# Optimization experiments

Hardware: AMD Instinct MI355X
Metric: run time of the kernel (lower is better)

The kernel has to match this reference:

```python
import jax, jax.numpy as jnp
import numpy as np

N = 100_000   # nodes
E = 1_600_000 # edges
D = 32        # input_channels
H = 32        # hidden_inputs
C = 8         # output_channels
G = 64        # graphs in batch


def setup_inputs() -> dict:
    key = jax.random.key(0)
    ks = jax.random.split(key, 12)
    inp = {
        "x": jax.random.normal(ks[0], (N, D), dtype=jnp.float32),
        "edge_idx": jax.random.randint(ks[1], (2, E), 0, N, dtype=jnp.int64 if jax.config.jax_enable_x64 else jnp.int32),
        "edge_weight": jax.random.uniform(ks[2], (E,), dtype=jnp.float32),
        "batch": jnp.sort(jax.random.randint(ks[3], (N,), 0, G, dtype=jnp.int32)),
        # GCNConv weights (PyG: out = A_hat @ (x W) + b)
        "W1": jax.random.normal(ks[4], (D, H), dtype=jnp.float32) / np.sqrt(D),
        "b1": jnp.zeros((H,), dtype=jnp.float32),
        "W2": jax.random.normal(ks[5], (H, H), dtype=jnp.float32) / np.sqrt(H),
        "b2": jnp.zeros((H,), dtype=jnp.float32),
        "W3": jax.random.normal(ks[6], (H, H), dtype=jnp.float32) / np.sqrt(H),
        "b3": jnp.zeros((H,), dtype=jnp.float32),
        "Wout": jax.random.normal(ks[7], (H, C), dtype=jnp.float32) / np.sqrt(H),
        "bout": jnp.zeros((C,), dtype=jnp.float32),
    }
    return inp


def _gcn_norm(edge_idx, edge_weight, n_nodes):
    """Add self-loops (weight 1) and compute symmetric normalization,
    matching torch_geometric gcn_norm(add_self_loops=True)."""
    loop = jnp.arange(n_nodes, dtype=edge_idx.dtype)
    row = jnp.concatenate([edge_idx[0], loop])          # source j
    col = jnp.concatenate([edge_idx[1], loop])          # target i
    w = jnp.concatenate([edge_weight, jnp.ones((n_nodes,), edge_weight.dtype)])
    deg = jax.ops.segment_sum(w, col, num_segments=n_nodes)  # in-degree of targets
    dinv = jnp.where(deg > 0, jax.lax.rsqrt(deg), 0.0)
    norm = dinv[row] * w * dinv[col]
    return row, col, norm


def _gcn_conv(x, W, b, row, col, norm, n_nodes):
    h = x @ W                                   # [N, H] small GEMM
    msg = h[row] * norm[:, None]                # gather + scale  [E+N, H]
    agg = jax.ops.segment_sum(msg, col, num_segments=n_nodes)  # scatter-add
    return agg + b


def reference(x, edge_idx, edge_weight, batch, W1, b1, W2, b2, W3, b3, Wout, bout):
    n = x.shape[0]
    row, col, norm = _gcn_norm(edge_idx, edge_weight, n)
    h = jax.nn.relu(_gcn_conv(x, W1, b1, row, col, norm, n))
    h = jax.nn.relu(_gcn_conv(h, W2, b2, row, col, norm, n))
    h = jax.nn.relu(_gcn_conv(h, W3, b3, row, col, norm, n))
    # global mean pool over graphs
    sums = jax.ops.segment_sum(h, batch, num_segments=G)          # [G, H]
    cnts = jax.ops.segment_sum(jnp.ones((n,), h.dtype), batch, num_segments=G)
    pooled = sums / jnp.maximum(cnts, 1.0)[:, None]
    # dropout is identity in eval mode
    logits = pooled @ Wout + bout
    return jax.nn.log_softmax(logits, axis=1)
```

## Files before the change

kernel.cpp:

```cpp
#include <hip/hip_runtime.h>
#include <math.h>

#define NN 100000
#define NE 1600000
#define HD 32
#define NG 64
#define NC 8

#define P 256
#define PART 391
#define SCAP 7000
#define CH 8192
#define NBIN ((NE + CH - 1) / CH)
#define NORM_BLOCKS (NN * 8 / 256)
#define GEMM0_BLOCKS (NN / 8)

__device__ __forceinline__ float bf2f(unsigned short u) {
    return __uint_as_float(((unsigned int)u) << 16);
}
__device__ __forceinline__ unsigned short f2bf(float f) {
    unsigned int b = __float_as_uint(f);
    b = (b + 0x7FFFu + ((b >> 16) & 1u)) >> 16;
    return (unsigned short)b;
}

#if __has_builtin(__builtin_amdgcn_cvt_pk_f32_fp8) && __has_builtin(__builtin_amdgcn_cvt_pk_fp8_f32)
#define FP8_HW 1
#else
#define FP8_HW 0
#endif

__device__ __forceinline__ float e4m3f_sw(unsigned u) {
    unsigned code = u & 0x7fu;
    unsigned e = code >> 3;
    float v;
    if (e == 0) v = (float)code * 0.001953125f;
    else v = __uint_as_float(((e + 120u) << 23) | ((code & 7u) << 20));
    return (u & 0x80u) ? -v : v;
}
__device__ __forceinline__ unsigned f2e4m3_sw(float f) {
    unsigned s = (__float_as_uint(f) >> 31) << 7;
    float a = fminf(fabsf(f), 448.0f);
    unsigned code;
    if (a >= 0.015625f) {
        unsigned x = __float_as_uint(a);
        x += 0x0007FFFFu + ((x >> 20) & 1u);
        code = (((x >> 23) - 120u) << 3) | ((x >> 20) & 7u);
    } else {
        code = (unsigned)__float2int_rn(a * 512.0f);
    }
    return s | code;
}

__device__ __forceinline__ float4 fp8x4f(unsigned v) {
#if FP8_HW
    using floatx2 = __attribute__((ext_vector_type(2))) float;
    floatx2 lo = __builtin_amdgcn_cvt_pk_f32_fp8((int)v, false);
    floatx2 hi = __builtin_amdgcn_cvt_pk_f32_fp8((int)v, true);
    return make_float4(lo[0], lo[1], hi[0], hi[1]);
#else
    return make_float4(e4m3f_sw(v & 255), e4m3f_sw((v >> 8) & 255),
                       e4m3f_sw((v >> 16) & 255), e4m3f_sw(v >> 24));
#endif
}
__device__ __forceinline__ unsigned f4fp8(float a, float b, float c, float d) {
#if FP8_HW
    int pk = 0;
    pk = __builtin_amdgcn_cvt_pk_fp8_f32(a, b, pk, false);
    pk = __builtin_amdgcn_cvt_pk_fp8_f32(c, d, pk, true);
    return (unsigned)pk;
#else
    return f2e4m3_sw(a) | (f2e4m3_sw(b) << 8) | (f2e4m3_sw(c) << 16) | (f2e4m3_sw(d) << 24);
#endif
}
__device__ __forceinline__ unsigned char f1fp8(float a) {
#if FP8_HW
    return (unsigned char)(__builtin_amdgcn_cvt_pk_fp8_f32(a, a, 0, false) & 0xff);
#else
    return (unsigned char)f2e4m3_sw(a);
#endif
}

__global__ __launch_bounds__(1024) void k_bin(const int* __restrict__ row,
                                              const int* __restrict__ col,
                                              const float* __restrict__ w,
                                              int* __restrict__ pcnt,
                                              uint2* __restrict__ staging) {
    __shared__ int scol[CH];
    __shared__ int hist[P];
    __shared__ int base_[P];
    int tid = threadIdx.x;
    int e0 = blockIdx.x * CH;
    int nrem = min(CH, NE - e0);
    if (tid < P) hist[tid] = 0;
    __syncthreads();
    for (int i = tid; i < nrem; i += 1024) {
        int c = col[e0 + i];
        scol[i] = c;
        atomicAdd(&hist[(unsigned)c / PART], 1);
    }
    __syncthreads();
    if (tid < P) {
        int h = hist[tid];
        base_[tid] = h ? atomicAdd(&pcnt[tid], h) : 0;
        hist[tid] = 0;
    }
    __syncthreads();
    for (int i = tid; i < nrem; i += 1024) {
        int c = scol[i];
        int p = (unsigned)c / PART;
        int pos = base_[p] + atomicAdd(&hist[p], 1);
        uint2 v;
        v.x = (unsigned)(c - p * PART) | ((unsigned)row[e0 + i] << 9);
        v.y = __float_as_uint(w[e0 + i]);
        staging[(size_t)p * SCAP + pos] = v;
    }
}

__global__ __launch_bounds__(256) void k_csrA_gemm0(const int* __restrict__ pcnt,
                                                    const uint2* __restrict__ staging,
                                                    int* __restrict__ off,
                                                    int* __restrict__ cntg,
                                                    float* __restrict__ dinv,
                                                    const float* __restrict__ x,
                                                    const float* __restrict__ W1,
                                                    unsigned char* __restrict__ h1) {
    int tid = threadIdx.x;
    if (blockIdx.x < P) {
        __shared__ int spc[P];
        __shared__ int cnt_l[PART];
        __shared__ float wsum[PART];
        __shared__ int sc[PART];
        int p = blockIdx.x;
        spc[tid] = pcnt[tid];
        __syncthreads();
#pragma unroll
        for (int d = 1; d < P; d <<= 1) {
            int t = (tid >= d) ? spc[tid - d] : 0;
            __syncthreads();
            spc[tid] += t;
            __syncthreads();
        }
        int m = pcnt[p];
        int pb = (p > 0) ? spc[p - 1] : 0;
        for (int i = tid; i < PART; i += 256) { cnt_l[i] = 0; wsum[i] = 0.0f; }
        __syncthreads();
        const uint2* st = staging + (size_t)p * SCAP;
        for (int i = tid; i < m; i += 256) {
            uint2 v = st[i];
            int cl = v.x & 511;
            atomicAdd(&cnt_l[cl], 1);
            atomicAdd(&wsum[cl], __uint_as_float(v.y));
        }
        __syncthreads();
        for (int i = tid; i < PART; i += 256) sc[i] = cnt_l[i];
        __syncthreads();
        int i0 = tid, i1 = tid + 256;
#pragma unroll
        for (int d = 1; d < 512; d <<= 1) {
            int t0 = 0, t1 = 0;
            if (i0 < PART && i0 >= d) t0 = sc[i0 - d];
            if (i1 < PART && i1 >= d) t1 = sc[i1 - d];
            __syncthreads();
            if (i0 < PART) sc[i0] += t0;
            if (i1 < PART) sc[i1] += t1;
            __syncthreads();
        }
        for (int i = tid; i < PART; i += 256) {
            int n = p * PART + i;
            if (n < NN) {
                off[n] = pb + sc[i] - cnt_l[i];
                cntg[n] = cnt_l[i];
                dinv[n] = rsqrtf(1.0f + wsum[i]);
            }
        }
    } else {
        __shared__ float sW[32 * 32];
        __shared__ float sX[8 * 32];
        int base = (blockIdx.x - P) * 8;
        ((float4*)sW)[tid] = ((const float4*)W1)[tid];
        if (tid < 64) ((float4*)sX)[tid] = ((const float4*)(x + (size_t)base * 32))[tid];
        __syncthreads();
        int c = tid & 31, nl = tid >> 5;
        float acc = 0.0f;
#pragma unroll
        for (int k = 0; k < 32; ++k) acc = fmaf(sX[nl * 32 + k], sW[k * 32 + c], acc);
        h1[(size_t)(base + nl) * 32 + c] = f1fp8(acc);
    }
}

__global__ __launch_bounds__(512) void k_csr_b(const int* __restrict__ pcnt,
                                               const uint2* __restrict__ staging,
                                               const int* __restrict__ off,
                                               const float* __restrict__ dinv,
                                               unsigned* __restrict__ pairs) {
    __shared__ int cur[PART];
    __shared__ float sdc[PART];
    int p = blockIdx.x, tid = threadIdx.x;
    int m = pcnt[p];
    const uint2* st = staging + (size_t)p * SCAP;
    for (int i = tid; i < PART; i += 512) {
        int n = p * PART + i;
        cur[i] = (n < NN) ? off[n] : 0;
        sdc[i] = (n < NN) ? dinv[n] : 0.0f;
    }
    __syncthreads();
    for (int ib = tid; ib < m; ib += 512 * 4) {
        uint2 v[4];
        float dr[4];
#pragma unroll
        for (int j = 0; j < 4; ++j) {
            int i = ib + j * 512;
            if (i < m) v[j] = st[i];
        }
#pragma unroll
        for (int j = 0; j < 4; ++j) {
            int i = ib + j * 512;
            if (i < m) dr[j] = dinv[v[j].x >> 9];
        }
#pragma unroll
        for (int j = 0; j < 4; ++j) {
            int i = ib + j * 512;
            if (i < m) {
                int cl = v[j].x & 511;
                int pos = atomicAdd(&cur[cl], 1);
                float y = dr[j] * __uint_as_float(v[j].y) * sdc[cl];
                unsigned q = (unsigned)__float2int_rn(y * 32768.0f);
                q = min(q, 32767u);
                pairs[pos] = ((v[j].x >> 9) << 15) | q;
            }
        }
    }
}

#define NM_SCALE 3.0517578125e-5f
template <int MODE>
__global__ __launch_bounds__(256) void k_gather(const unsigned char* __restrict__ hb,
                                                const int* __restrict__ off,
                                                const int* __restrict__ cntg,
                                                const float* __restrict__ dinv,
                                                const unsigned* __restrict__ pairs,
                                                const float* __restrict__ bias,
                                                const float* __restrict__ Wn,
                                                unsigned char* __restrict__ hout,
                                                unsigned short* __restrict__ h3out) {
    __shared__ float sW[32 * 32];
    __shared__ float srow[32 * 33];
    int tid = threadIdx.x;
    if (MODE == 0) ((float4*)sW)[tid] = ((const float4*)Wn)[tid];
    int t = blockIdx.x * 256 + tid;
    int n = t >> 3, c4 = t & 7;
    int cn = cntg[n];
    const unsigned* pp = pairs + off[n];
    float di = dinv[n], sl = di * di;
    unsigned hu = *(const unsigned*)(hb + (size_t)n * 32 + c4 * 4);
    float4 hf = fp8x4f(hu);
    float4 acc = make_float4(sl * hf.x, sl * hf.y, sl * hf.z, sl * hf.w);
    int k = 0;
    for (; k + 8 <= cn; k += 8) {
        unsigned p[8];
#pragma unroll
        for (int j = 0; j < 8; ++j) p[j] = pp[k + j];
        unsigned v[8];
#pragma unroll
        for (int j = 0; j < 8; ++j)
            v[j] = *(const unsigned*)(hb + (size_t)(p[j] >> 15) * 32 + c4 * 4);
#pragma unroll
        for (int j = 0; j < 8; ++j) {
            float nm = (float)(p[j] & 32767u) * NM_SCALE;
            float4 f = fp8x4f(v[j]);
            acc.x = fmaf(nm, f.x, acc.x);
            acc.y = fmaf(nm, f.y, acc.y);
            acc.z = fmaf(nm, f.z, acc.z);
            acc.w = fmaf(nm, f.w, acc.w);
        }
    }
    for (; k + 4 <= cn; k += 4) {
        unsigned p[4];
#pragma unroll
        for (int j = 0; j < 4; ++j) p[j] = pp[k + j];
        unsigned v[4];
#pragma unroll
        for (int j = 0; j < 4; ++j)
            v[j] = *(const unsigned*)(hb + (size_t)(p[j] >> 15) * 32 + c4 * 4);
#pragma unroll
        for (int j = 0; j < 4; ++j) {
            float nm = (float)(p[j] & 32767u) * NM_SCALE;
            float4 f = fp8x4f(v[j]);
            acc.x = fmaf(nm, f.x, acc.x);
            acc.y = fmaf(nm, f.y, acc.y);
            acc.z = fmaf(nm, f.z, acc.z);
            acc.w = fmaf(nm, f.w, acc.w);
        }
    }
    for (; k < cn; ++k) {
        unsigned p = pp[k];
        unsigned v = *(const unsigned*)(hb + (size_t)(p >> 15) * 32 + c4 * 4);
        float nm = (float)(p & 32767u) * NM_SCALE;
        float4 f = fp8x4f(v);
        acc.x = fmaf(nm, f.x, acc.x);
        acc.y = fmaf(nm, f.y, acc.y);
        acc.z = fmaf(nm, f.z, acc.z);
        acc.w = fmaf(nm, f.w, acc.w);
    }
    int cb = c4 * 4;
    if (MODE == 0) {
        int ln = tid >> 3;
        srow[ln * 33 + cb + 0] = fmaxf(acc.x + bias[cb + 0], 0.0f);
        srow[ln * 33 + cb + 1] = fmaxf(acc.y + bias[cb + 1], 0.0f);
        srow[ln * 33 + cb + 2] = fmaxf(acc.z + bias[cb + 2], 0.0f);
        srow[ln * 33 + cb + 3] = fmaxf(acc.w + bias[cb + 3], 0.0f);
        __syncthreads();
        const float* rw = srow + ln * 33;
        float o0 = 0.f, o1 = 0.f, o2 = 0.f, o3 = 0.f;
#pragma unroll
        for (int kk = 0; kk < 32; ++kk) {
            float r = rw[kk];
            const float* wr = sW + kk * 32 + cb;
            o0 = fmaf(r, wr[0], o0);
            o1 = fmaf(r, wr[1], o1);
            o2 = fmaf(r, wr[2], o2);
            o3 = fmaf(r, wr[3], o3);
        }
        *(unsigned*)(hout + (size_t)n * 32 + cb) = f4fp8(o0, o1, o2, o3);
    } else {
        ushort4 ou;
        ou.x = f2bf(fmaxf(acc.x + bias[cb + 0], 0.0f));
        ou.y = f2bf(fmaxf(acc.y + bias[cb + 1], 0.0f));
        ou.z = f2bf(fmaxf(acc.z + bias[cb + 2], 0.0f));
        ou.w = f2bf(fmaxf(acc.w + bias[cb + 3], 0.0f));
        *((ushort4*)(h3out + (size_t)n * 32) + c4) = ou;
    }
}

__global__ __launch_bounds__(1024) void k_pool_head(const unsigned short* __restrict__ h3,
                                                    const int* __restrict__ batch,
                                                    const float* __restrict__ Wout,
                                                    const float* __restrict__ bout,
                                                    float* __restrict__ out) {
    int g = blockIdx.x;
    __shared__ int sb[2];
    if (threadIdx.x == 0) {
        int lo = 0, hi = NN;
        while (lo < hi) { int m = (lo + hi) >> 1; if (batch[m] < g) lo = m + 1; else hi = m; }
        sb[0] = lo;
        lo = 0; hi = NN;
        while (lo < hi) { int m = (lo + hi) >> 1; if (batch[m] < g + 1) lo = m + 1; else hi = m; }
        sb[1] = lo;
    }
    __syncthreads();
    int start = sb[0], end = sb[1];
    int c = threadIdx.x & 31, grp = threadIdx.x >> 5;
    float acc = 0.0f;
    for (int n = start + grp; n < end; n += 32)
        acc += bf2f(h3[(size_t)n * 32 + c]);
    __shared__ float red[32 * 32];
    red[grp * 32 + c] = acc;
    __syncthreads();
    __shared__ float pooled[32];
    if (threadIdx.x < 32) {
        float s = 0.0f;
#pragma unroll
        for (int gr = 0; gr < 32; ++gr) s += red[gr * 32 + threadIdx.x];
        pooled[threadIdx.x] = s / fmaxf((float)(end - start), 1.0f);
    }
    __syncthreads();
    __shared__ float slog[8];
    if (threadIdx.x < 8) {
        float l = bout[threadIdx.x];
#pragma unroll
        for (int k = 0; k < 32; ++k) l = fmaf(pooled[k], Wout[k * 8 + threadIdx.x], l);
        slog[threadIdx.x] = l;
    }
    __syncthreads();
    if (threadIdx.x < 8) {
        float m = slog[0];
#pragma unroll
        for (int i = 1; i < 8; ++i) m = fmaxf(m, slog[i]);
        float s = 0.0f;
#pragma unroll
        for (int i = 0; i < 8; ++i) s += expf(slog[i] - m);
        out[g * NC + threadIdx.x] = slog[threadIdx.x] - m - logf(s);
    }
}

extern "C" void kernel_launch(void* const* d_in, const int* in_sizes, int n_in,
                              void* d_out, int out_size, void* d_ws, size_t ws_size,
                              hipStream_t stream) {
    const float* x     = (const float*)d_in[0];
    const int*   eidx  = (const int*)d_in[1];
    const float* ew    = (const float*)d_in[2];
    const int*   batch = (const int*)d_in[3];
    const float* W1 = (const float*)d_in[4];
    const float* b1 = (const float*)d_in[5];
    const float* W2 = (const float*)d_in[6];
    const float* b2 = (const float*)d_in[7];
    const float* W3 = (const float*)d_in[8];
    const float* b3 = (const float*)d_in[9];
    const float* Wout = (const float*)d_in[10];
    const float* bout = (const float*)d_in[11];
    float* out = (float*)d_out;

    const int* row = eidx;
    const int* col = eidx + NE;

    unsigned char* h1 = (unsigned char*)d_ws;
    unsigned char* h2 = h1 + (size_t)NN * HD;
    unsigned short* h3 = (unsigned short*)(h2 + (size_t)NN * HD);
    unsigned* pairs = (unsigned*)(h3 + (size_t)NN * HD);
    uint2* staging = (uint2*)(pairs + NE);
    float* dinv = (float*)(staging + (size_t)P * SCAP);
    int* off  = (int*)(dinv + NN);
    int* cntg = off + NN;
    int* pcnt = cntg + NN;

    hipMemsetAsync(pcnt, 0, P * sizeof(int), stream);
    k_bin<<<NBIN, 1024, 0, stream>>>(row, col, ew, pcnt, staging);
    k_csrA_gemm0<<<P + GEMM0_BLOCKS, 256, 0, stream>>>(pcnt, staging, off, cntg, dinv,
                                                       x, W1, h1);
    k_csr_b<<<P, 512, 0, stream>>>(pcnt, staging, off, dinv, pairs);
    k_gather<0><<<NORM_BLOCKS, 256, 0, stream>>>(h1, off, cntg, dinv, pairs, b1, W2,
                                                 h2, nullptr);
    k_gather<0><<<NORM_BLOCKS, 256, 0, stream>>>(h2, off, cntg, dinv, pairs, b2, W3,
                                                 h1, nullptr);
    k_gather<1><<<NORM_BLOCKS, 256, 0, stream>>>(h1, off, cntg, dinv, pairs, b3, nullptr,
                                                 nullptr, h3);
    k_pool_head<<<NG, 1024, 0, stream>>>(h3, batch, Wout, bout, out);
}
```

Before: 134.2 us.

## Fold GCN normalization into node features and merge CSR build kernels

Moves the first-layer GEMM into the binning kernel and merges the two CSR construction kernels into one, cutting one launch and the off/dinv round trip. Edge weights are now stored raw in the pairs list, and the source-side dinv is pre-multiplied into the node features (h1 scaled in k_csr, outputs scaled by di in gather). This removes the random dinv gather per edge. In exchange it adds a bf16 temporary stage for h1 and keeps the staging pass inside one kernel per partition, which may reduce parallelism.

```diff
diff --git a/kernel.cpp b/kernel.cpp
--- a/kernel.cpp
+++ b/kernel.cpp
@@ -12,8 +12,8 @@
 #define SCAP 7000
 #define CH 8192
 #define NBIN ((NE + CH - 1) / CH)
+#define GEMM0_BLOCKS32 (NN / 32)
 #define NORM_BLOCKS (NN * 8 / 256)
-#define GEMM0_BLOCKS (NN / 8)
 
 __device__ __forceinline__ float bf2f(unsigned short u) {
     return __uint_as_float(((unsigned int)u) << 16);
@@ -73,150 +73,135 @@
     return f2e4m3_sw(a) | (f2e4m3_sw(b) << 8) | (f2e4m3_sw(c) << 16) | (f2e4m3_sw(d) << 24);
 #endif
 }
-__device__ __forceinline__ unsigned char f1fp8(float a) {
-#if FP8_HW
-    return (unsigned char)(__builtin_amdgcn_cvt_pk_fp8_f32(a, a, 0, false) & 0xff);
-#else
-    return (unsigned char)f2e4m3_sw(a);
-#endif
-}
-
-__global__ __launch_bounds__(1024) void k_bin(const int* __restrict__ row,
-                                              const int* __restrict__ col,
-                                              const float* __restrict__ w,
-                                              int* __restrict__ pcnt,
-                                              uint2* __restrict__ staging) {
-    __shared__ int scol[CH];
-    __shared__ int hist[P];
-    __shared__ int base_[P];
-    int tid = threadIdx.x;
-    int e0 = blockIdx.x * CH;
-    int nrem = min(CH, NE - e0);
-    if (tid < P) hist[tid] = 0;
-    __syncthreads();
-    for (int i = tid; i < nrem; i += 1024) {
-        int c = col[e0 + i];
-        scol[i] = c;
-        atomicAdd(&hist[(unsigned)c / PART], 1);
-    }
-    __syncthreads();
-    if (tid < P) {
-        int h = hist[tid];
-        base_[tid] = h ? atomicAdd(&pcnt[tid], h) : 0;
-        hist[tid] = 0;
-    }
-    __syncthreads();
-    for (int i = tid; i < nrem; i += 1024) {
-        int c = scol[i];
-        int p = (unsigned)c / PART;
-        int pos = base_[p] + atomicAdd(&hist[p], 1);
-        uint2 v;
-        v.x = (unsigned)(c - p * PART) | ((unsigned)row[e0 + i] << 9);
-        v.y = __float_as_uint(w[e0 + i]);
-        staging[(size_t)p * SCAP + pos] = v;
-    }
-}
-
-__global__ __launch_bounds__(256) void k_csrA_gemm0(const int* __restrict__ pcnt,
-                                                    const uint2* __restrict__ staging,
-                                                    int* __restrict__ off,
-                                                    int* __restrict__ cntg,
-                                                    float* __restrict__ dinv,
+
+__global__ __launch_bounds__(1024) void k_bin_gemm0(const int* __restrict__ row,
+                                                    const int* __restrict__ col,
+                                                    const float* __restrict__ w,
+                                                    int* __restrict__ pcnt,
+                                                    uint2* __restrict__ staging,
                                                     const float* __restrict__ x,
                                                     const float* __restrict__ W1,
-                                                    unsigned char* __restrict__ h1) {
+                                                    unsigned short* __restrict__ htmp) {
     int tid = threadIdx.x;
-    if (blockIdx.x < P) {
-        __shared__ int spc[P];
-        __shared__ int cnt_l[PART];
-        __shared__ float wsum[PART];
-        __shared__ int sc[PART];
-        int p = blockIdx.x;
-        spc[tid] = pcnt[tid];
-        __syncthreads();
-#pragma unroll
-        for (int d = 1; d < P; d <<= 1) {
-            int t = (tid >= d) ? spc[tid - d] : 0;
-            __syncthreads();
-            spc[tid] += t;
-            __syncthreads();
-        }
-        int m = pcnt[p];
-        int pb = (p > 0) ? spc[p - 1] : 0;
-        for (int i = tid; i < PART; i += 256) { cnt_l[i] = 0; wsum[i] = 0.0f; }
-        __syncthreads();
-        const uint2* st = staging + (size_t)p * SCAP;
-        for (int i = tid; i < m; i += 256) {
-            uint2 v = st[i];
-            int cl = v.x & 511;
-            atomicAdd(&cnt_l[cl], 1);
-            atomicAdd(&wsum[cl], __uint_as_float(v.y));
-        }
-        __syncthreads();
-        for (int i = tid; i < PART; i += 256) sc[i] = cnt_l[i];
-        __syncthreads();
-        int i0 = tid, i1 = tid + 256;
-#pragma unroll
-        for (int d = 1; d < 512; d <<= 1) {
-            int t0 = 0, t1 = 0;
-            if (i0 < PART && i0 >= d) t0 = sc[i0 - d];
-            if (i1 < PART && i1 >= d) t1 = sc[i1 - d];
-            __syncthreads();
-            if (i0 < PART) sc[i0] += t0;
-            if (i1 < PART) sc[i1] += t1;
-            __syncthreads();
-        }
-        for (int i = tid; i < PART; i += 256) {
-            int n = p * PART + i;
-            if (n < NN) {
-                off[n] = pb + sc[i] - cnt_l[i];
-                cntg[n] = cnt_l[i];
-                dinv[n] = rsqrtf(1.0f + wsum[i]);
-            }
+    if (blockIdx.x < NBIN) {
+        __shared__ int hist[P];
+        __shared__ int base_[P];
+        int e0 = blockIdx.x * CH;
+        int nrem = min(CH, NE - e0);
+        if (tid < P) hist[tid] = 0;
+        __syncthreads();
+        for (int i = tid; i < nrem; i += 1024)
+            atomicAdd(&hist[(unsigned)col[e0 + i] / PART], 1);
+        __syncthreads();
+        if (tid < P) {
+            int h = hist[tid];
+            base_[tid] = h ? atomicAdd(&pcnt[tid], h) : 0;
+            hist[tid] = 0;
+        }
+        __syncthreads();
+        for (int i = tid; i < nrem; i += 1024) {
+            int c = col[e0 + i];
+            int p = (unsigned)c / PART;
+            int pos = base_[p] + atomicAdd(&hist[p], 1);
+            uint2 v;
+            v.x = (unsigned)(c - p * PART) | ((unsigned)row[e0 + i] << 9);
+            v.y = __float_as_uint(w[e0 + i]);
+            staging[(size_t)p * SCAP + pos] = v;
         }
     } else {
         __shared__ float sW[32 * 32];
-        __shared__ float sX[8 * 32];
-        int base = (blockIdx.x - P) * 8;
-        ((float4*)sW)[tid] = ((const float4*)W1)[tid];
-        if (tid < 64) ((float4*)sX)[tid] = ((const float4*)(x + (size_t)base * 32))[tid];
-        __syncthreads();
-        int c = tid & 31, nl = tid >> 5;
+        __shared__ float sX[32 * 32];
+        int base = (blockIdx.x - NBIN) * 32;
+        if (tid < 256) {
+            ((float4*)sW)[tid] = ((const float4*)W1)[tid];
+            ((float4*)sX)[tid] = ((const float4*)(x + (size_t)base * 32))[tid];
+        }
+        __syncthreads();
+        int nl = tid >> 5, c = tid & 31;
         float acc = 0.0f;
 #pragma unroll
         for (int k = 0; k < 32; ++k) acc = fmaf(sX[nl * 32 + k], sW[k * 32 + c], acc);
-        h1[(size_t)(base + nl) * 32 + c] = f1fp8(acc);
-    }
-}
-
-__global__ __launch_bounds__(512) void k_csr_b(const int* __restrict__ pcnt,
-                                               const uint2* __restrict__ staging,
-                                               const int* __restrict__ off,
-                                               const float* __restrict__ dinv,
-                                               unsigned* __restrict__ pairs) {
+        htmp[(size_t)(base + nl) * 32 + c] = f2bf(acc);
+    }
+}
+
+__global__ __launch_bounds__(512) void k_csr(const int* __restrict__ pcnt,
+                                             const uint2* __restrict__ staging,
+                                             int* __restrict__ off,
+                                             int* __restrict__ cntg,
+                                             float* __restrict__ dinv,
+                                             const unsigned short* __restrict__ htmp,
+                                             unsigned char* __restrict__ h1,
+                                             unsigned* __restrict__ pairs) {
+    __shared__ int spc[P];
+    __shared__ int cnt_l[PART];
+    __shared__ float wsum[PART];
+    __shared__ int sc[PART];
+    __shared__ float sdc[PART];
     __shared__ int cur[PART];
-    __shared__ float sdc[PART];
     int p = blockIdx.x, tid = threadIdx.x;
+    if (tid < P) spc[tid] = pcnt[tid];
+    __syncthreads();
+#pragma unroll
+    for (int d = 1; d < P; d <<= 1) {
+        int t = 0;
+        if (tid < P && tid >= d) t = spc[tid - d];
+        __syncthreads();
+        if (tid < P) spc[tid] += t;
+        __syncthreads();
+    }
     int m = pcnt[p];
+    int pb = (p > 0) ? spc[p - 1] : 0;
+    for (int i = tid; i < PART; i += 512) { cnt_l[i] = 0; wsum[i] = 0.0f; }
+    __syncthreads();
     const uint2* st = staging + (size_t)p * SCAP;
+    for (int i = tid; i < m; i += 512) {
+        uint2 v = st[i];
+        int cl = v.x & 511;
+        atomicAdd(&cnt_l[cl], 1);
+        atomicAdd(&wsum[cl], __uint_as_float(v.y));
+    }
+    __syncthreads();
+    for (int i = tid; i < PART; i += 512) sc[i] = cnt_l[i];
+    __syncthreads();
+#pragma unroll
+    for (int d = 1; d < 512; d <<= 1) {
+        int t = 0;
+        if (tid < PART && tid >= d) t = sc[tid - d];
+        __syncthreads();
+        if (tid < PART) sc[tid] += t;
+        __syncthreads();
+    }
     for (int i = tid; i < PART; i += 512) {
+        int excl = sc[i] - cnt_l[i];
+        cur[i] = excl;
+        float dv = rsqrtf(1.0f + wsum[i]);
+        sdc[i] = dv;
         int n = p * PART + i;
-        cur[i] = (n < NN) ? off[n] : 0;
-        sdc[i] = (n < NN) ? dinv[n] : 0.0f;
-    }
-    __syncthreads();
+        if (n < NN) {
+            off[n] = pb + excl;
+            cntg[n] = cnt_l[i];
+            dinv[n] = dv;
+        }
+    }
+    __syncthreads();
+    for (int u = tid; u < PART * 8; u += 512) {
+        int i = u >> 3, q = u & 7;
+        int n = p * PART + i;
+        if (n < NN) {
+            ushort4 hv = *((const ushort4*)(htmp + (size_t)n * 32) + q);
+            float dv = sdc[i];
+            *(unsigned*)(h1 + (size_t)n * 32 + q * 4) =
+                f4fp8(dv * bf2f(hv.x), dv * bf2f(hv.y), dv * bf2f(hv.z), dv * bf2f(hv.w));
+        }
+    }
+    unsigned* pr = pairs + pb;
     for (int ib = tid; ib < m; ib += 512 * 4) {
         uint2 v[4];
-        float dr[4];
 #pragma unroll
         for (int j = 0; j < 4; ++j) {
             int i = ib + j * 512;
             if (i < m) v[j] = st[i];
-        }
-#pragma unroll
-        for (int j = 0; j < 4; ++j) {
-            int i = ib + j * 512;
-            if (i < m) dr[j] = dinv[v[j].x >> 9];
         }
 #pragma unroll
         for (int j = 0; j < 4; ++j) {
@@ -224,10 +209,9 @@
             if (i < m) {
                 int cl = v[j].x & 511;
                 int pos = atomicAdd(&cur[cl], 1);
-                float y = dr[j] * __uint_as_float(v[j].y) * sdc[cl];
-                unsigned q = (unsigned)__float2int_rn(y * 32768.0f);
+                unsigned q = (unsigned)__float2int_rn(__uint_as_float(v[j].y) * 32768.0f);
                 q = min(q, 32767u);
-                pairs[pos] = ((v[j].x >> 9) << 15) | q;
+                pr[pos] = ((v[j].x >> 9) << 15) | q;
             }
         }
     }
@@ -252,10 +236,9 @@
     int n = t >> 3, c4 = t & 7;
     int cn = cntg[n];
     const unsigned* pp = pairs + off[n];
-    float di = dinv[n], sl = di * di;
+    float di = dinv[n];
     unsigned hu = *(const unsigned*)(hb + (size_t)n * 32 + c4 * 4);
-    float4 hf = fp8x4f(hu);
-    float4 acc = make_float4(sl * hf.x, sl * hf.y, sl * hf.z, sl * hf.w);
+    float4 acc = fp8x4f(hu);
     int k = 0;
     for (; k + 8 <= cn; k += 8) {
         unsigned p[8];
@@ -306,10 +289,10 @@
     int cb = c4 * 4;
     if (MODE == 0) {
         int ln = tid >> 3;
-        srow[ln * 33 + cb + 0] = fmaxf(acc.x + bias[cb + 0], 0.0f);
-        srow[ln * 33 + cb + 1] = fmaxf(acc.y + bias[cb + 1], 0.0f);
-        srow[ln * 33 + cb + 2] = fmaxf(acc.z + bias[cb + 2], 0.0f);
-        srow[ln * 33 + cb + 3] = fmaxf(acc.w + bias[cb + 3], 0.0f);
+        srow[ln * 33 + cb + 0] = fmaxf(fmaf(di, acc.x, bias[cb + 0]), 0.0f);
+        srow[ln * 33 + cb + 1] = fmaxf(fmaf(di, acc.y, bias[cb + 1]), 0.0f);
+        srow[ln * 33 + cb + 2] = fmaxf(fmaf(di, acc.z, bias[cb + 2]), 0.0f);
+        srow[ln * 33 + cb + 3] = fmaxf(fmaf(di, acc.w, bias[cb + 3]), 0.0f);
         __syncthreads();
         const float* rw = srow + ln * 33;
         float o0 = 0.f, o1 = 0.f, o2 = 0.f, o3 = 0.f;
@@ -322,13 +305,13 @@
             o2 = fmaf(r, wr[2], o2);
             o3 = fmaf(r, wr[3], o3);
         }
-        *(unsigned*)(hout + (size_t)n * 32 + cb) = f4fp8(o0, o1, o2, o3);
+        *(unsigned*)(hout + (size_t)n * 32 + cb) = f4fp8(di * o0, di * o1, di * o2, di * o3);
     } else {
         ushort4 ou;
-        ou.x = f2bf(fmaxf(acc.x + bias[cb + 0], 0.0f));
-        ou.y = f2bf(fmaxf(acc.y + bias[cb + 1], 0.0f));
-        ou.z = f2bf(fmaxf(acc.z + bias[cb + 2], 0.0f));
-        ou.w = f2bf(fmaxf(acc.w + bias[cb + 3], 0.0f));
+        ou.x = f2bf(fmaxf(fmaf(di, acc.x, bias[cb + 0]), 0.0f));
+        ou.y = f2bf(fmaxf(fmaf(di, acc.y, bias[cb + 1]), 0.0f));
+        ou.z = f2bf(fmaxf(fmaf(di, acc.z, bias[cb + 2]), 0.0f));
+        ou.w = f2bf(fmaxf(fmaf(di, acc.w, bias[cb + 3]), 0.0f));
         *((ushort4*)(h3out + (size_t)n * 32) + c4) = ou;
     }
 }
@@ -415,10 +398,9 @@
     int* pcnt = cntg + NN;
 
     hipMemsetAsync(pcnt, 0, P * sizeof(int), stream);
-    k_bin<<<NBIN, 1024, 0, stream>>>(row, col, ew, pcnt, staging);
-    k_csrA_gemm0<<<P + GEMM0_BLOCKS, 256, 0, stream>>>(pcnt, staging, off, cntg, dinv,
-                                                       x, W1, h1);
-    k_csr_b<<<P, 512, 0, stream>>>(pcnt, staging, off, dinv, pairs);
+    k_bin_gemm0<<<NBIN + GEMM0_BLOCKS32, 1024, 0, stream>>>(row, col, ew, pcnt, staging,
+                                                            x, W1, h3 );
+    k_csr<<<P, 512, 0, stream>>>(pcnt, staging, off, cntg, dinv, h3 , h1, pairs);
     k_gather<0><<<NORM_BLOCKS, 256, 0, stream>>>(h1, off, cntg, dinv, pairs, b1, W2,
                                                  h2, nullptr);
     k_gather<0><<<NORM_BLOCKS, 256, 0, stream>>>(h2, off, cntg, dinv, pairs, b2, W3,
```

Result: faster. 126.2 us (-5.9%).
